# Kernel optimization log

Measured on AMD Instinct MI355X. Metric: run time of the kernel, lower is better.

The kernel has to match this reference:

```python
import jax, jax.numpy as jnp
import numpy as np

B, N, HID, NH = 8, 1024, 1024, 16
HD = HID // NH  # head_dim = 64
MLP = 4 * HID
EPS = 1e-6


def _xavier(key, fan_in, fan_out):
    lim = np.sqrt(6.0 / (fan_in + fan_out))
    return jax.random.uniform(key, (fan_in, fan_out), jnp.float32, -lim, lim)


def setup_inputs() -> dict:
    key = jax.random.key(0)
    ks = jax.random.split(key, 10)
    return {
        "x": jax.random.normal(ks[0], (B, N, HID), jnp.float32),
        "c": jax.random.normal(ks[1], (B, HID), jnp.float32),
        "w_ada": _xavier(ks[2], HID, 6 * HID), "b_ada": jnp.zeros((6 * HID,), jnp.float32),
        "wq": _xavier(ks[3], HID, HID), "bq": jnp.zeros((HID,), jnp.float32),
        "wk": _xavier(ks[4], HID, HID), "bk": jnp.zeros((HID,), jnp.float32),
        "wv": _xavier(ks[5], HID, HID), "bv": jnp.zeros((HID,), jnp.float32),
        "wo": _xavier(ks[6], HID, HID), "bo": jnp.zeros((HID,), jnp.float32),
        "w1": _xavier(ks[7], HID, MLP), "b1": jnp.zeros((MLP,), jnp.float32),
        "w2": _xavier(ks[8], MLP, HID), "b2": jnp.zeros((HID,), jnp.float32),
    }


def _ln(t):
    # LayerNorm, elementwise_affine=False, eps=1e-6
    mu = jnp.mean(t, axis=-1, keepdims=True)
    var = jnp.mean(jnp.square(t - mu), axis=-1, keepdims=True)
    return (t - mu) * jax.lax.rsqrt(var + EPS)


def _modulate(t, shift, scale):
    return t * (1.0 + scale[:, None, :]) + shift[:, None, :]


def reference(x, c, w_ada, b_ada, wq, bq, wk, bk, wv, bv, wo, bo, w1, b1, w2, b2):
    cmod = jax.nn.silu(c) @ w_ada + b_ada  # [B, 6*HID]
    sh_msa, sc_msa, g_msa, sh_mlp, sc_mlp, g_mlp = jnp.split(cmod, 6, axis=-1)

    xm = _modulate(_ln(x), sh_msa, sc_msa)  # [B, N, HID]
    q = (xm @ wq + bq).reshape(B, N, NH, HD)
    k = (xm @ wk + bk).reshape(B, N, NH, HD)
    v = (xm @ wv + bv).reshape(B, N, NH, HD)

    # NOTE: original scales by 1/head_dim (not 1/sqrt(head_dim)), fp32 softmax
    scores = jnp.einsum('bihd,bjhd->bhij', q, k) / HD
    attn = jax.nn.softmax(scores.astype(jnp.float32), axis=-1)
    out = jnp.einsum('bhij,bjhd->bihd', attn, v).astype(v.dtype)
    out = out.reshape(B, N, HID) @ wo + bo

    x = x + g_msa[:, None, :] * out

    xm2 = _modulate(_ln(x), sh_mlp, sc_mlp)
    h = jax.nn.gelu(xm2 @ w1 + b1, approximate=False)  # nn.GELU default = exact
    mlp_out = h @ w2 + b2
    return x + g_mlp[:, None, :] * mlp_out
```

## Files before the change

kernel.cpp:

```cpp
#include <hip/hip_runtime.h>
#include <hip/hip_bf16.h>
#include <cstdint>


typedef __bf16 bf16;
typedef __attribute__((ext_vector_type(8))) __bf16 bf16x8;
typedef __attribute__((ext_vector_type(4))) __bf16 bf16x4;
typedef __attribute__((ext_vector_type(4))) float f32x4;

#define SEQ   1024
#define NHID  1024
#define NHEAD 16
#define HDIM  64
#define CMS   6144

#define GLD16(gp, lp)                                                  \
  __builtin_amdgcn_global_load_lds(                                    \
      (const __attribute__((address_space(1))) void*)(gp),             \
      (__attribute__((address_space(3))) void*)(lp), 16, 0, 0)

template <int N> __device__ __forceinline__ void vmwait() {
  if constexpr (N == 0)      asm volatile("s_waitcnt vmcnt(0)" ::: "memory");
  else if constexpr (N == 4) asm volatile("s_waitcnt vmcnt(4)" ::: "memory");
  else if constexpr (N == 6) asm volatile("s_waitcnt vmcnt(6)" ::: "memory");
}

#define BAR()                                                          \
  { asm volatile("" ::: "memory");                                     \
    __builtin_amdgcn_s_barrier();                                      \
    asm volatile("" ::: "memory"); }

#define LGKM0() asm volatile("s_waitcnt lgkmcnt(0)" ::: "memory")

struct TP4 { const float* s[4]; bf16* d[4]; };

__global__ __launch_bounds__(256) void transpose_conv4(TP4 p)
{
  __shared__ float tile[32][33];
  const float* __restrict__ src = p.s[blockIdx.z];
  bf16* __restrict__ dst = p.d[blockIdx.z];
  int n0 = blockIdx.x * 32, k0 = blockIdx.y * 32;
  int tx = threadIdx.x & 31, ty = threadIdx.x >> 5;
#pragma unroll
  for (int i = 0; i < 32; i += 8)
    tile[ty + i][tx] = src[(size_t)(k0 + ty + i) * 1024 + n0 + tx];
  __syncthreads();
#pragma unroll
  for (int i = 0; i < 32; i += 8)
    dst[(size_t)(n0 + ty + i) * 1024 + k0 + tx] = (bf16)tile[tx][ty + i];
}

__global__ __launch_bounds__(256) void transpose_conv(
    const float* __restrict__ src, bf16* __restrict__ dst, int K, int N)
{
  __shared__ float tile[32][33];
  int n0 = blockIdx.x * 32, k0 = blockIdx.y * 32;
  int tx = threadIdx.x & 31, ty = threadIdx.x >> 5;
#pragma unroll
  for (int i = 0; i < 32; i += 8)
    tile[ty + i][tx] = src[(size_t)(k0 + ty + i) * N + n0 + tx];
  __syncthreads();
#pragma unroll
  for (int i = 0; i < 32; i += 8)
    dst[(size_t)(n0 + ty + i) * K + k0 + tx] = (bf16)tile[tx][ty + i];
}

__global__ __launch_bounds__(256) void ada_kernel(
    const float* __restrict__ c, const float* __restrict__ w_ada,
    const float* __restrict__ b_ada, float* __restrict__ cmod)
{
  __shared__ float cs[1024];
  int b = blockIdx.y;
  int col = blockIdx.x * 256 + threadIdx.x;
  for (int i = threadIdx.x; i < 1024; i += 256) {
    float cv = c[b * 1024 + i];
    cs[i] = cv / (1.0f + __expf(-cv));
  }
  __syncthreads();
  float acc = b_ada[col];
#pragma unroll 8
  for (int kk = 0; kk < 1024; kk++)
    acc += cs[kk] * w_ada[(size_t)kk * CMS + col];
  cmod[b * CMS + col] = acc;
}

__global__ __launch_bounds__(256) void ln_mod(
    const float* __restrict__ x, const float* __restrict__ cmod,
    bf16* __restrict__ out, int sh_off, int sc_off)
{
  int row = blockIdx.x, b = row >> 10, tid = threadIdx.x;
  const float4* xr = (const float4*)(x + (size_t)row * NHID);
  float4 v = xr[tid];
  float s  = v.x + v.y + v.z + v.w;
  float s2 = v.x * v.x + v.y * v.y + v.z * v.z + v.w * v.w;
#pragma unroll
  for (int off = 32; off; off >>= 1) {
    s  += __shfl_xor(s, off);
    s2 += __shfl_xor(s2, off);
  }
  __shared__ float red1[4], red2[4];
  int wave = tid >> 6, lane = tid & 63;
  if (lane == 0) { red1[wave] = s; red2[wave] = s2; }
  __syncthreads();
  float S  = red1[0] + red1[1] + red1[2] + red1[3];
  float S2 = red2[0] + red2[1] + red2[2] + red2[3];
  float mean = S * (1.0f / NHID);
  float var  = S2 * (1.0f / NHID) - mean * mean;
  float rs   = rsqrtf(var + 1e-6f);
  const float4* shp = (const float4*)(cmod + b * CMS + sh_off);
  const float4* scp = (const float4*)(cmod + b * CMS + sc_off);
  float4 sh4 = shp[tid], sc4 = scp[tid];
  bf16x4 o4;
  o4[0] = (bf16)((v.x - mean) * rs * (1.0f + sc4.x) + sh4.x);
  o4[1] = (bf16)((v.y - mean) * rs * (1.0f + sc4.y) + sh4.y);
  o4[2] = (bf16)((v.z - mean) * rs * (1.0f + sc4.z) + sh4.z);
  o4[3] = (bf16)((v.w - mean) * rs * (1.0f + sc4.w) + sh4.w);
  *(bf16x4*)(out + (size_t)row * NHID + tid * 4) = o4;
}

template <int EPI, int BN>
__global__ __launch_bounds__(512, 2) void gemm8(
    const bf16* __restrict__ A, const bf16* __restrict__ Bt,
    const float* __restrict__ bias, const float* __restrict__ bias2,
    const float* __restrict__ bias3,
    bf16* __restrict__ outb, bf16* __restrict__ outb2,
    bf16* __restrict__ outb3, float* __restrict__ outf,
    const float* __restrict__ cmod, int gate_off,
    const float* __restrict__ resid,
    int N, int K)
{
  constexpr int BNH   = BN / 2;
  constexpr int LB    = BNH / 64;
  constexpr int MF    = BN / 64;
  constexpr int WC    = BN / 64;
  constexpr int WRS   = 256 / (8 / WC) / 2;
  constexpr int VMN   = (LB == 2) ? 6 : 4;
  constexpr int BOFF  = 65536;
  constexpr int BBUF  = BNH * 256;
  constexpr int BHALF = BNH * 128;

  extern __shared__ __align__(16) char smem[];

  const int tid  = threadIdx.x;
  const int xcd  = blockIdx.x & 7;
  const int slot = blockIdx.x >> 3;
  const int by   = xcd * 4 + (slot & 3);
  const int bx   = slot >> 2;
  const int bm = by * 256, bn = bx * BN;

  const int wave = tid >> 6, lane = tid & 63;
  const int wr = wave / WC, wc = wave % WC;
  const int l16 = lane & 15, q4 = lane >> 4;

  const int rq = tid >> 3;
  const int ch = ((tid & 7) ^ (rq & 7)) * 8;
  const int wbase = (tid & 448) * 16;

  const int aRowB = (wr * WRS + l16) * 128;
  const int bRowB = (wc * 32 + l16) * 128;
  const int slotB = (q4 ^ (l16 & 7)) * 16;

  f32x4 acc[2][2][MF][2];
#pragma unroll
  for (int a0 = 0; a0 < 2; a0++)
#pragma unroll
    for (int a1 = 0; a1 < 2; a1++)
#pragma unroll
      for (int a2 = 0; a2 < MF; a2++)
#pragma unroll
        for (int a3 = 0; a3 < 2; a3++) acc[a0][a1][a2][a3] = (f32x4)0.0f;

  auto stA = [&](int buf, int half, int T) {
    const bf16* g = A + (size_t)(bm + half * 128 + rq) * K + T * 64 + ch;
    char* l = smem + buf * 32768 + half * 16384 + wbase;
    GLD16(g, l);
    GLD16(g + (size_t)64 * K, l + 8192);
  };
  auto stB = [&](int buf, int half, int T) {
    const bf16* g = Bt + (size_t)(bn + half * BNH + rq) * K + T * 64 + ch;
    char* l = smem + BOFF + buf * BBUF + half * BHALF + wbase;
    GLD16(g, l);
    if constexpr (LB == 2) { GLD16(g + (size_t)64 * K, l + 8192); }
  };

#define RDA(BUF, QM, FR)                                                   \
  { const char* ab_ = smem + (BUF) * 32768 + (QM) * 16384 + aRowB;         \
    _Pragma("unroll")                                                      \
    for (int ks = 0; ks < 2; ks++) {                                       \
      const int sb_ = slotB ^ (ks * 64);                                   \
      _Pragma("unroll")                                                    \
      for (int mf = 0; mf < MF; mf++)                                      \
        FR[ks][mf] = *(const bf16x8*)(ab_ + mf * 2048 + sb_);              \
    } }

#define RDB(BUF, QN, FR)                                                   \
  { const char* bb_ = smem + BOFF + (BUF) * BBUF + (QN) * BHALF + bRowB;   \
    _Pragma("unroll")                                                      \
    for (int ks = 0; ks < 2; ks++) {                                       \
      const int sb_ = slotB ^ (ks * 64);                                   \
      _Pragma("unroll")                                                    \
      for (int nf = 0; nf < 2; nf++)                                       \
        FR[ks][nf] = *(const bf16x8*)(bb_ + nf * 2048 + sb_);              \
    } }

#define MM(QM, QN, AF, BF)                                                 \
  { __builtin_amdgcn_s_setprio(1);                                         \
    _Pragma("unroll")                                                      \
    for (int mf = 0; mf < MF; mf++)                                        \
      _Pragma("unroll")                                                    \
      for (int nf = 0; nf < 2; nf++) {                                     \
        acc[QM][QN][mf][nf] = __builtin_amdgcn_mfma_f32_16x16x32_bf16(     \
            AF[0][mf], BF[0][nf], acc[QM][QN][mf][nf], 0, 0, 0);           \
        acc[QM][QN][mf][nf] = __builtin_amdgcn_mfma_f32_16x16x32_bf16(     \
            AF[1][mf], BF[1][nf], acc[QM][QN][mf][nf], 0, 0, 0);           \
      }                                                                    \
    __builtin_amdgcn_s_setprio(0); }

  const int NT = K >> 6, NI = NT >> 1;

  bf16x8 afr[2][MF], bfr0[2][2], bfr1[2][2];

  stA(0, 0, 0); stB(0, 0, 0); stB(0, 1, 0); stA(0, 1, 0);
  stA(1, 0, 1); stB(1, 0, 1); stB(1, 1, 1);
  vmwait<VMN>();
  BAR();

  for (int i = 0; i < NI; ++i) {
    const int t = 2 * i;
    const int u2 = (t + 2 < NT) ? t + 2 : NT - 2;
    const int u3 = (t + 3 < NT) ? t + 3 : NT - 1;
    RDA(0, 0, afr); RDB(0, 0, bfr0);
    stA(1, 1, t + 1);
    BAR(); LGKM0();
    MM(0, 0, afr, bfr0);
    BAR();
    RDB(0, 1, bfr1);
    stA(0, 0, u2);
    BAR(); LGKM0();
    MM(0, 1, afr, bfr1);
    BAR();
    RDA(0, 1, afr);
    stB(0, 0, u2);
    BAR(); LGKM0();
    MM(1, 1, afr, bfr1);
    BAR();
    stB(0, 1, u2);
    vmwait<VMN>();
    BAR();
    MM(1, 0, afr, bfr0);
    BAR();
    RDA(1, 0, afr); RDB(1, 0, bfr0);
    stA(0, 1, u2);
    BAR(); LGKM0();
    MM(0, 0, afr, bfr0);
    BAR();
    RDB(1, 1, bfr1);
    stA(1, 0, u3);
    BAR(); LGKM0();
    MM(0, 1, afr, bfr1);
    BAR();
    RDA(1, 1, afr);
    stB(1, 0, u3);
    BAR(); LGKM0();
    MM(1, 1, afr, bfr1);
    BAR();
    stB(1, 1, u3);
    vmwait<VMN>();
    BAR();
    MM(1, 0, afr, bfr0);
    BAR();
  }
  vmwait<0>();
#undef RDA
#undef RDB
#undef MM

  const int colBase = bn + wc * 32 + l16;
  const int rowBase = bm + wr * WRS + q4 * 4;
#pragma unroll
  for (int qm = 0; qm < 2; qm++)
#pragma unroll
  for (int qn = 0; qn < 2; qn++)
#pragma unroll
  for (int mf = 0; mf < MF; mf++)
#pragma unroll
  for (int nf = 0; nf < 2; nf++) {
    const int col  = colBase + qn * BNH + nf * 16;
    const int row0 = rowBase + qm * 128 + mf * 16;
    f32x4 v = acc[qm][qn][mf][nf];
    if constexpr (EPI == 5) {
      const int sel = bn >> 10;
      const float* bp = (sel == 0) ? bias : (sel == 1) ? bias2 : bias3;
      const int colq = col & 1023;
      const float bcol = bp[colq];
      if (sel == 2) {
        bf16x4 o4;
#pragma unroll
        for (int r = 0; r < 4; r++) o4[r] = (bf16)(v[r] + bcol);
        const int bidx = row0 >> 10;
        *(bf16x4*)(outb3 + ((size_t)bidx * NHID + colq) * SEQ +
                   (row0 & 1023)) = o4;
      } else {
        bf16* qk = (sel == 0) ? outb : outb2;
#pragma unroll
        for (int r = 0; r < 4; r++)
          qk[(size_t)(row0 + r) * 1024 + colq] = (bf16)(v[r] + bcol);
      }
    } else if constexpr (EPI == 2) {
      const float bcol = bias[col];
#pragma unroll
      for (int r = 0; r < 4; r++) {
        float val = v[r] + bcol;
        float u2g = 2.0f * val * (0.7978845608f + 0.0356774081f * val * val);
        float e = __expf(u2g);
        float th = 1.0f - 2.0f / (e + 1.0f);
        outb[(size_t)(row0 + r) * N + col] = (bf16)(0.5f * val * (1.0f + th));
      }
    } else {
      const float bcol = bias[col];
#pragma unroll
      for (int r = 0; r < 4; r++) {
        const int row = row0 + r;
        const float gg = cmod[(row >> 10) * CMS + gate_off + col];
        outf[(size_t)row * N + col] =
            resid[(size_t)row * N + col] + gg * (v[r] + bcol);
      }
    }
  }
}

__global__ __launch_bounds__(512) void attn_mfma(
    const bf16* __restrict__ q, const bf16* __restrict__ k,
    const bf16* __restrict__ vt, bf16* __restrict__ o)
{
  __shared__ __align__(16) bf16 Ks[64 * 64];
  __shared__ __align__(16) bf16 Vs[64 * 64];
  __shared__ __align__(16) bf16 Ps[8][32 * 72];

  int bid = blockIdx.x;
  int qt = bid & 3, h = (bid >> 2) & 15, b = bid >> 6;
  int tid = threadIdx.x, wave = tid >> 6, lane = tid & 63;
  int quad = lane >> 4, l16 = lane & 15;
  int qbase = qt * 256 + wave * 32;

  bf16x8 qf[2][2];
  const bf16* qp = q + ((size_t)(b * SEQ + qbase)) * NHID + h * HDIM;
#pragma unroll
  for (int nt = 0; nt < 2; nt++)
#pragma unroll
    for (int kk = 0; kk < 2; kk++) {
      bf16x8 t = *(const bf16x8*)(qp + (size_t)(nt * 16 + l16) * NHID +
                                  kk * 32 + quad * 8);
#pragma unroll
      for (int j = 0; j < 8; j++) t[j] = (bf16)((float)t[j] * 0.015625f);
      qf[nt][kk] = t;
    }

  f32x4 oacc[4][2];
#pragma unroll
  for (int mt = 0; mt < 4; mt++)
#pragma unroll
    for (int nt = 0; nt < 2; nt++) oacc[mt][nt] = (f32x4)0.0f;
  float m_[2] = {-3.0e38f, -3.0e38f}, l_[2] = {0.0f, 0.0f};

  const bf16* kb = k + ((size_t)(b * SEQ)) * NHID + h * HDIM;
  const bf16* vb = vt + ((size_t)(b * NHID + h * HDIM)) * SEQ;

  const int sr0 = tid >> 3, sc0 = tid & 7;
  const int cg0 = (sc0 ^ (sr0 & 7)) * 8;
  bf16* lk0 = Ks + (size_t)(tid & 448) * 8;
  bf16* lv0 = Vs + (size_t)(tid & 448) * 8;

  for (int kt = 0; kt < 16; kt++) {
    __syncthreads();
    GLD16(kb + (size_t)(kt * 64 + sr0) * NHID + cg0, lk0);
    GLD16(vb + (size_t)sr0 * SEQ + kt * 64 + cg0, lv0);
    __syncthreads();

    f32x4 sacc[4][2];
#pragma unroll
    for (int mt = 0; mt < 4; mt++)
#pragma unroll
      for (int nt = 0; nt < 2; nt++) sacc[mt][nt] = (f32x4)0.0f;
#pragma unroll
    for (int kk = 0; kk < 2; kk++) {
      bf16x8 kf[4];
#pragma unroll
      for (int mt = 0; mt < 4; mt++) {
        int row = mt * 16 + l16;
        kf[mt] = *(const bf16x8*)(Ks + row * 64 +
                                  (((kk * 4 + quad) ^ (row & 7)) * 8));
      }
#pragma unroll
      for (int mt = 0; mt < 4; mt++)
#pragma unroll
        for (int nt = 0; nt < 2; nt++)
          sacc[mt][nt] = __builtin_amdgcn_mfma_f32_16x16x32_bf16(
              kf[mt], qf[nt][kk], sacc[mt][nt], 0, 0, 0);
    }

    float alpha[2];
#pragma unroll
    for (int nt = 0; nt < 2; nt++) {
      float tm = -3.0e38f;
#pragma unroll
      for (int mt = 0; mt < 4; mt++)
#pragma unroll
        for (int r = 0; r < 4; r++) tm = fmaxf(tm, sacc[mt][nt][r]);
      tm = fmaxf(tm, __shfl_xor(tm, 16));
      tm = fmaxf(tm, __shfl_xor(tm, 32));
      float mn = fmaxf(m_[nt], tm);
      alpha[nt] = __expf(m_[nt] - mn);
      m_[nt] = mn;
      float ts = 0.0f;
#pragma unroll
      for (int mt = 0; mt < 4; mt++) {
        bf16x4 pv;
#pragma unroll
        for (int r = 0; r < 4; r++) {
          float p = __expf(sacc[mt][nt][r] - mn);
          ts += p;
          pv[r] = (bf16)p;
        }
        *(bf16x4*)(&Ps[wave][(nt * 16 + l16) * 72 + mt * 16 + quad * 4]) = pv;
      }
      ts += __shfl_xor(ts, 16);
      ts += __shfl_xor(ts, 32);
      l_[nt] = l_[nt] * alpha[nt] + ts;
    }
#pragma unroll
    for (int mt = 0; mt < 4; mt++)
#pragma unroll
      for (int nt = 0; nt < 2; nt++)
#pragma unroll
        for (int r = 0; r < 4; r++) oacc[mt][nt][r] *= alpha[nt];

    __asm__ volatile("s_waitcnt lgkmcnt(0)" ::: "memory");

#pragma unroll
    for (int kk = 0; kk < 2; kk++) {
      bf16x8 vf[4], pf[2];
#pragma unroll
      for (int mt = 0; mt < 4; mt++) {
        int row = mt * 16 + l16;
        vf[mt] = *(const bf16x8*)(Vs + row * 64 +
                                  (((kk * 4 + quad) ^ (row & 7)) * 8));
      }
#pragma unroll
      for (int nt = 0; nt < 2; nt++)
        pf[nt] = *(const bf16x8*)(&Ps[wave][(nt * 16 + l16) * 72 +
                                            kk * 32 + quad * 8]);
#pragma unroll
      for (int mt = 0; mt < 4; mt++)
#pragma unroll
        for (int nt = 0; nt < 2; nt++)
          oacc[mt][nt] = __builtin_amdgcn_mfma_f32_16x16x32_bf16(
              vf[mt], pf[nt], oacc[mt][nt], 0, 0, 0);
    }
  }

#pragma unroll
  for (int nt = 0; nt < 2; nt++) {
    float rl = 1.0f / l_[nt];
#pragma unroll
    for (int mt = 0; mt < 4; mt++) {
      bf16x4 o4;
#pragma unroll
      for (int r = 0; r < 4; r++) o4[r] = (bf16)(oacc[mt][nt][r] * rl);
      *(bf16x4*)(o + ((size_t)(b * SEQ + qbase + nt * 16 + l16)) * NHID +
                 h * HDIM + mt * 16 + quad * 4) = o4;
    }
  }
}

#define OFF_CMOD 0u
#define OFF_WQT  196608u
#define OFF_WKT  (OFF_WQT + 2097152u)
#define OFF_WVT  (OFF_WKT + 2097152u)
#define OFF_WOT  (OFF_WVT + 2097152u)
#define OFF_W1T  (OFF_WOT + 2097152u)
#define OFF_W2T  (OFF_W1T + 8388608u)
#define OFF_X2   (OFF_W2T + 8388608u)
#define OFF_XM2  (OFF_X2  + 33554432u)
#define OFF_POOL (OFF_XM2 + 16777216u)

extern "C" void kernel_launch(void* const* d_in, const int* in_sizes, int n_in,
                              void* d_out, int out_size, void* d_ws, size_t ws_size,
                              hipStream_t stream)
{
  const float* x     = (const float*)d_in[0];
  const float* c     = (const float*)d_in[1];
  const float* w_ada = (const float*)d_in[2];
  const float* b_ada = (const float*)d_in[3];
  const float* wq = (const float*)d_in[4];  const float* bq = (const float*)d_in[5];
  const float* wk = (const float*)d_in[6];  const float* bk = (const float*)d_in[7];
  const float* wv = (const float*)d_in[8];  const float* bv = (const float*)d_in[9];
  const float* wo = (const float*)d_in[10]; const float* bo = (const float*)d_in[11];
  const float* w1 = (const float*)d_in[12]; const float* b1 = (const float*)d_in[13];
  const float* w2 = (const float*)d_in[14]; const float* b2 = (const float*)d_in[15];
  float* out = (float*)d_out;
  char* ws = (char*)d_ws;

  float* cmod = (float*)(ws + OFF_CMOD);
  bf16* wqT = (bf16*)(ws + OFF_WQT);
  bf16* wkT = (bf16*)(ws + OFF_WKT);
  bf16* wvT = (bf16*)(ws + OFF_WVT);
  bf16* woT = (bf16*)(ws + OFF_WOT);
  bf16* w1T = (bf16*)(ws + OFF_W1T);
  bf16* w2T = (bf16*)(ws + OFF_W2T);
  float* x2 = (float*)(ws + OFF_X2);
  bf16* xm2 = (bf16*)(ws + OFF_XM2);
  bf16* xm  = (bf16*)(ws + OFF_POOL);
  bf16* qb  = (bf16*)(ws + OFF_POOL + 16777216u);
  bf16* kb  = (bf16*)(ws + OFF_POOL + 33554432u);
  bf16* vtb = (bf16*)(ws + OFF_POOL + 50331648u);
  bf16* ob  = xm;
  bf16* hb  = xm;

  static bool attr_set = false;
  if (!attr_set) {
    hipFuncSetAttribute(reinterpret_cast<const void*>(&gemm8<5, 128>),
                        hipFuncAttributeMaxDynamicSharedMemorySize, 98304);
    hipFuncSetAttribute(reinterpret_cast<const void*>(&gemm8<1, 128>),
                        hipFuncAttributeMaxDynamicSharedMemorySize, 98304);
    hipFuncSetAttribute(reinterpret_cast<const void*>(&gemm8<2, 256>),
                        hipFuncAttributeMaxDynamicSharedMemorySize, 131072);
    hipFuncSetAttribute(reinterpret_cast<const void*>(&gemm8<3, 128>),
                        hipFuncAttributeMaxDynamicSharedMemorySize, 98304);
    attr_set = true;
  }

  TP4 tp;
  tp.s[0] = wq; tp.s[1] = wk; tp.s[2] = wv; tp.s[3] = wo;
  tp.d[0] = wqT; tp.d[1] = wkT; tp.d[2] = wvT; tp.d[3] = woT;
  transpose_conv4<<<dim3(32, 32, 4), 256, 0, stream>>>(tp);
  transpose_conv<<<dim3(128, 32), 256, 0, stream>>>(w1, w1T, 1024, 4096);
  transpose_conv<<<dim3(32, 128), 256, 0, stream>>>(w2, w2T, 4096, 1024);

  ada_kernel<<<dim3(24, 8), 256, 0, stream>>>(c, w_ada, b_ada, cmod);

  ln_mod<<<8192, 256, 0, stream>>>(x, cmod, xm, 0, 1024);

  gemm8<5, 128><<<768, 512, 98304, stream>>>(
      xm, wqT, bq, bk, bv, qb, kb, vtb, nullptr, nullptr, 0, nullptr,
      1024, 1024);

  attn_mfma<<<512, 512, 0, stream>>>(qb, kb, vtb, ob);

  gemm8<1, 128><<<256, 512, 98304, stream>>>(
      ob, woT, bo, nullptr, nullptr, nullptr, nullptr, nullptr, x2,
      cmod, 2048, x, 1024, 1024);

  ln_mod<<<8192, 256, 0, stream>>>(x2, cmod, xm2, 3072, 4096);

  gemm8<2, 256><<<512, 512, 131072, stream>>>(
      xm2, w1T, b1, nullptr, nullptr, hb, nullptr, nullptr, nullptr,
      nullptr, 0, nullptr, 4096, 1024);

  gemm8<3, 128><<<256, 512, 98304, stream>>>(
      hb, w2T, b2, nullptr, nullptr, nullptr, nullptr, nullptr, out,
      cmod, 5120, x2, 1024, 4096);
}
```

Measured before the change: 542.6 us.

## Simplify GEMM pipeline to per-tile double buffer and drop BN=256 variant

The GEMM kernel drops its BN template parameter and its finely interleaved 8-phase ping-pong schedule. It now uses a simpler loop that processes one K-tile per iteration, does a full buffer reload with two barriers per tile, and always uses a 256x128 tile. The MLP up-projection now launches 1024 blocks of the smaller tile instead of 512 blocks of 256x256, using less shared memory. This trades the finer overlap of loads and MFMA work, plus the higher reuse of the larger tile, for simpler code and more blocks.

After: 551.1 us. No clear change (+1.6%).

```diff
diff --git a/kernel.cpp b/kernel.cpp
--- a/kernel.cpp
+++ b/kernel.cpp
@@ -21,7 +21,6 @@
 
 template <int N> __device__ __forceinline__ void vmwait() {
   if constexpr (N == 0)      asm volatile("s_waitcnt vmcnt(0)" ::: "memory");
-  else if constexpr (N == 4) asm volatile("s_waitcnt vmcnt(4)" ::: "memory");
   else if constexpr (N == 6) asm volatile("s_waitcnt vmcnt(6)" ::: "memory");
 }
 
@@ -118,7 +117,7 @@
   *(bf16x4*)(out + (size_t)row * NHID + tid * 4) = o4;
 }
 
-template <int EPI, int BN>
+template <int EPI>
 __global__ __launch_bounds__(512, 2) void gemm8(
     const bf16* __restrict__ A, const bf16* __restrict__ Bt,
     const float* __restrict__ bias, const float* __restrict__ bias2,
@@ -129,15 +128,7 @@
     const float* __restrict__ resid,
     int N, int K)
 {
-  constexpr int BNH   = BN / 2;
-  constexpr int LB    = BNH / 64;
-  constexpr int MF    = BN / 64;
-  constexpr int WC    = BN / 64;
-  constexpr int WRS   = 256 / (8 / WC) / 2;
-  constexpr int VMN   = (LB == 2) ? 6 : 4;
-  constexpr int BOFF  = 65536;
-  constexpr int BBUF  = BNH * 256;
-  constexpr int BHALF = BNH * 128;
+  constexpr int BOFF = 65536;
 
   extern __shared__ __align__(16) char smem[];
 
@@ -146,55 +137,54 @@
   const int slot = blockIdx.x >> 3;
   const int by   = xcd * 4 + (slot & 3);
   const int bx   = slot >> 2;
-  const int bm = by * 256, bn = bx * BN;
+  const int bm = by * 256, bn = bx * 128;
 
   const int wave = tid >> 6, lane = tid & 63;
-  const int wr = wave / WC, wc = wave % WC;
+  const int wr = wave >> 1, wc = wave & 1;
   const int l16 = lane & 15, q4 = lane >> 4;
 
   const int rq = tid >> 3;
   const int ch = ((tid & 7) ^ (rq & 7)) * 8;
   const int wbase = (tid & 448) * 16;
 
-  const int aRowB = (wr * WRS + l16) * 128;
+  const int aRowB = (wr * 32 + l16) * 128;
   const int bRowB = (wc * 32 + l16) * 128;
   const int slotB = (q4 ^ (l16 & 7)) * 16;
 
-  f32x4 acc[2][2][MF][2];
+  f32x4 acc[2][2][2][2];
 #pragma unroll
   for (int a0 = 0; a0 < 2; a0++)
 #pragma unroll
     for (int a1 = 0; a1 < 2; a1++)
 #pragma unroll
-      for (int a2 = 0; a2 < MF; a2++)
+      for (int a2 = 0; a2 < 2; a2++)
 #pragma unroll
         for (int a3 = 0; a3 < 2; a3++) acc[a0][a1][a2][a3] = (f32x4)0.0f;
 
-  auto stA = [&](int buf, int half, int T) {
+  auto stA = [&](int p, int half, int T) {
     const bf16* g = A + (size_t)(bm + half * 128 + rq) * K + T * 64 + ch;
-    char* l = smem + buf * 32768 + half * 16384 + wbase;
+    char* l = smem + p * 32768 + half * 16384 + wbase;
     GLD16(g, l);
     GLD16(g + (size_t)64 * K, l + 8192);
   };
-  auto stB = [&](int buf, int half, int T) {
-    const bf16* g = Bt + (size_t)(bn + half * BNH + rq) * K + T * 64 + ch;
-    char* l = smem + BOFF + buf * BBUF + half * BHALF + wbase;
+  auto stB = [&](int p, int half, int T) {
+    const bf16* g = Bt + (size_t)(bn + half * 64 + rq) * K + T * 64 + ch;
+    char* l = smem + BOFF + p * 16384 + half * 8192 + wbase;
     GLD16(g, l);
-    if constexpr (LB == 2) { GLD16(g + (size_t)64 * K, l + 8192); }
   };
 
-#define RDA(BUF, QM, FR)                                                   \
-  { const char* ab_ = smem + (BUF) * 32768 + (QM) * 16384 + aRowB;         \
+#define RDA(P, QM, FR)                                                     \
+  { const char* ab_ = smem + (P) * 32768 + (QM) * 16384 + aRowB;           \
     _Pragma("unroll")                                                      \
     for (int ks = 0; ks < 2; ks++) {                                       \
       const int sb_ = slotB ^ (ks * 64);                                   \
       _Pragma("unroll")                                                    \
-      for (int mf = 0; mf < MF; mf++)                                      \
+      for (int mf = 0; mf < 2; mf++)                                       \
         FR[ks][mf] = *(const bf16x8*)(ab_ + mf * 2048 + sb_);              \
     } }
 
-#define RDB(BUF, QN, FR)                                                   \
-  { const char* bb_ = smem + BOFF + (BUF) * BBUF + (QN) * BHALF + bRowB;   \
+#define RDB(P, QN, FR)                                                     \
+  { const char* bb_ = smem + BOFF + (P) * 16384 + (QN) * 8192 + bRowB;     \
     _Pragma("unroll")                                                      \
     for (int ks = 0; ks < 2; ks++) {                                       \
       const int sb_ = slotB ^ (ks * 64);                                   \
@@ -206,7 +196,7 @@
 #define MM(QM, QN, AF, BF)                                                 \
   { __builtin_amdgcn_s_setprio(1);                                         \
     _Pragma("unroll")                                                      \
-    for (int mf = 0; mf < MF; mf++)                                        \
+    for (int mf = 0; mf < 2; mf++)                                         \
       _Pragma("unroll")                                                    \
       for (int nf = 0; nf < 2; nf++) {                                     \
         acc[QM][QN][mf][nf] = __builtin_amdgcn_mfma_f32_16x16x32_bf16(     \
@@ -216,59 +206,28 @@
       }                                                                    \
     __builtin_amdgcn_s_setprio(0); }
 
-  const int NT = K >> 6, NI = NT >> 1;
-
-  bf16x8 afr[2][MF], bfr0[2][2], bfr1[2][2];
+  const int NT = K >> 6;
+
+  bf16x8 afr[2][2], bfr0[2][2], bfr1[2][2];
 
   stA(0, 0, 0); stB(0, 0, 0); stB(0, 1, 0); stA(0, 1, 0);
-  stA(1, 0, 1); stB(1, 0, 1); stB(1, 1, 1);
-  vmwait<VMN>();
+  stA(1, 0, 1); stB(1, 0, 1); stB(1, 1, 1); stA(1, 1, 1);
+  vmwait<6>();
   BAR();
 
-  for (int i = 0; i < NI; ++i) {
-    const int t = 2 * i;
-    const int u2 = (t + 2 < NT) ? t + 2 : NT - 2;
-    const int u3 = (t + 3 < NT) ? t + 3 : NT - 1;
-    RDA(0, 0, afr); RDB(0, 0, bfr0);
-    stA(1, 1, t + 1);
-    BAR(); LGKM0();
-    MM(0, 0, afr, bfr0);
+  for (int t = 0; t < NT; ++t) {
+    const int p = t & 1;
+    const int T = (t + 2 < NT) ? t + 2 : t;
+    RDA(p, 0, afr); RDB(p, 0, bfr0); RDB(p, 1, bfr1);
+    LGKM0();
+    MM(0, 0, afr, bfr0); MM(0, 1, afr, bfr1);
+    RDA(p, 1, afr);
+    LGKM0();
     BAR();
-    RDB(0, 1, bfr1);
-    stA(0, 0, u2);
-    BAR(); LGKM0();
-    MM(0, 1, afr, bfr1);
+    stA(p, 0, T); stB(p, 0, T); stB(p, 1, T); stA(p, 1, T);
+    vmwait<6>();
     BAR();
-    RDA(0, 1, afr);
-    stB(0, 0, u2);
-    BAR(); LGKM0();
-    MM(1, 1, afr, bfr1);
-    BAR();
-    stB(0, 1, u2);
-    vmwait<VMN>();
-    BAR();
-    MM(1, 0, afr, bfr0);
-    BAR();
-    RDA(1, 0, afr); RDB(1, 0, bfr0);
-    stA(0, 1, u2);
-    BAR(); LGKM0();
-    MM(0, 0, afr, bfr0);
-    BAR();
-    RDB(1, 1, bfr1);
-    stA(1, 0, u3);
-    BAR(); LGKM0();
-    MM(0, 1, afr, bfr1);
-    BAR();
-    RDA(1, 1, afr);
-    stB(1, 0, u3);
-    BAR(); LGKM0();
-    MM(1, 1, afr, bfr1);
-    BAR();
-    stB(1, 1, u3);
-    vmwait<VMN>();
-    BAR();
-    MM(1, 0, afr, bfr0);
-    BAR();
+    MM(1, 1, afr, bfr1); MM(1, 0, afr, bfr0);
   }
   vmwait<0>();
 #undef RDA
@@ -276,16 +235,16 @@
 #undef MM
 
   const int colBase = bn + wc * 32 + l16;
-  const int rowBase = bm + wr * WRS + q4 * 4;
+  const int rowBase = bm + wr * 32 + q4 * 4;
 #pragma unroll
   for (int qm = 0; qm < 2; qm++)
 #pragma unroll
   for (int qn = 0; qn < 2; qn++)
 #pragma unroll
-  for (int mf = 0; mf < MF; mf++)
+  for (int mf = 0; mf < 2; mf++)
 #pragma unroll
   for (int nf = 0; nf < 2; nf++) {
-    const int col  = colBase + qn * BNH + nf * 16;
+    const int col  = colBase + qn * 64 + nf * 16;
     const int row0 = rowBase + qm * 128 + mf * 16;
     f32x4 v = acc[qm][qn][mf][nf];
     if constexpr (EPI == 5) {
@@ -519,13 +478,13 @@
 
   static bool attr_set = false;
   if (!attr_set) {
-    hipFuncSetAttribute(reinterpret_cast<const void*>(&gemm8<5, 128>),
+    hipFuncSetAttribute(reinterpret_cast<const void*>(&gemm8<5>),
                         hipFuncAttributeMaxDynamicSharedMemorySize, 98304);
-    hipFuncSetAttribute(reinterpret_cast<const void*>(&gemm8<1, 128>),
+    hipFuncSetAttribute(reinterpret_cast<const void*>(&gemm8<1>),
                         hipFuncAttributeMaxDynamicSharedMemorySize, 98304);
-    hipFuncSetAttribute(reinterpret_cast<const void*>(&gemm8<2, 256>),
-                        hipFuncAttributeMaxDynamicSharedMemorySize, 131072);
-    hipFuncSetAttribute(reinterpret_cast<const void*>(&gemm8<3, 128>),
+    hipFuncSetAttribute(reinterpret_cast<const void*>(&gemm8<2>),
+                        hipFuncAttributeMaxDynamicSharedMemorySize, 98304);
+    hipFuncSetAttribute(reinterpret_cast<const void*>(&gemm8<3>),
                         hipFuncAttributeMaxDynamicSharedMemorySize, 98304);
     attr_set = true;
   }
@@ -541,23 +500,23 @@
 
   ln_mod<<<8192, 256, 0, stream>>>(x, cmod, xm, 0, 1024);
 
-  gemm8<5, 128><<<768, 512, 98304, stream>>>(
+  gemm8<5><<<768, 512, 98304, stream>>>(
       xm, wqT, bq, bk, bv, qb, kb, vtb, nullptr, nullptr, 0, nullptr,
       1024, 1024);
 
   attn_mfma<<<512, 512, 0, stream>>>(qb, kb, vtb, ob);
 
-  gemm8<1, 128><<<256, 512, 98304, stream>>>(
+  gemm8<1><<<256, 512, 98304, stream>>>(
       ob, woT, bo, nullptr, nullptr, nullptr, nullptr, nullptr, x2,
       cmod, 2048, x, 1024, 1024);
 
   ln_mod<<<8192, 256, 0, stream>>>(x2, cmod, xm2, 3072, 4096);
 
-  gemm8<2, 256><<<512, 512, 131072, stream>>>(
+  gemm8<2><<<1024, 512, 98304, stream>>>(
       xm2, w1T, b1, nullptr, nullptr, hb, nullptr, nullptr, nullptr,
       nullptr, 0, nullptr, 4096, 1024);
 
-  gemm8<3, 128><<<256, 512, 98304, stream>>>(
+  gemm8<3><<<256, 512, 98304, stream>>>(
       hb, w2T, b2, nullptr, nullptr, nullptr, nullptr, nullptr, out,
       cmod, 5120, x2, 1024, 4096);
 }
```

## Double-buffer K/V tiles in attention and split-K the adaLN projection

Applied to the files above, without the earlier changes.

The attention kernel now keeps two LDS buffers for the K and V tiles. It issues the async global-to-LDS load for the next key tile before computing on the current one, and drops one of the two per-iteration barriers. The adaLN modulation GEMV is split four ways along K across a new grid dimension and accumulated with float atomics into a buffer zeroed by a memset. This raises block count for that small kernel. The cost is extra LDS per attention block, an additional memset launch, and non-deterministic summation order in cmod.

New measurement: 503.1 us. 1.08x faster.

```diff
diff --git a/kernel.cpp b/kernel.cpp
--- a/kernel.cpp
+++ b/kernel.cpp
@@ -69,19 +69,20 @@
     const float* __restrict__ c, const float* __restrict__ w_ada,
     const float* __restrict__ b_ada, float* __restrict__ cmod)
 {
-  __shared__ float cs[1024];
-  int b = blockIdx.y;
-  int col = blockIdx.x * 256 + threadIdx.x;
-  for (int i = threadIdx.x; i < 1024; i += 256) {
-    float cv = c[b * 1024 + i];
-    cs[i] = cv / (1.0f + __expf(-cv));
+  __shared__ float cs[256];
+  const int b  = blockIdx.y;
+  const int k0 = blockIdx.z * 256;
+  const int col = blockIdx.x * 256 + threadIdx.x;
+  {
+    float cv = c[b * 1024 + k0 + threadIdx.x];
+    cs[threadIdx.x] = cv / (1.0f + __expf(-cv));
   }
   __syncthreads();
-  float acc = b_ada[col];
+  float acc = (blockIdx.z == 0) ? b_ada[col] : 0.0f;
 #pragma unroll 8
-  for (int kk = 0; kk < 1024; kk++)
-    acc += cs[kk] * w_ada[(size_t)kk * CMS + col];
-  cmod[b * CMS + col] = acc;
+  for (int kk = 0; kk < 256; kk++)
+    acc += cs[kk] * w_ada[(size_t)(k0 + kk) * CMS + col];
+  atomicAdd(&cmod[b * CMS + col], acc);
 }
 
 __global__ __launch_bounds__(256) void ln_mod(
@@ -333,8 +334,8 @@
     const bf16* __restrict__ q, const bf16* __restrict__ k,
     const bf16* __restrict__ vt, bf16* __restrict__ o)
 {
-  __shared__ __align__(16) bf16 Ks[64 * 64];
-  __shared__ __align__(16) bf16 Vs[64 * 64];
+  __shared__ __align__(16) bf16 Ks[2][64 * 64];
+  __shared__ __align__(16) bf16 Vs[2][64 * 64];
   __shared__ __align__(16) bf16 Ps[8][32 * 72];
 
   int bid = blockIdx.x;
@@ -368,14 +369,19 @@
 
   const int sr0 = tid >> 3, sc0 = tid & 7;
   const int cg0 = (sc0 ^ (sr0 & 7)) * 8;
-  bf16* lk0 = Ks + (size_t)(tid & 448) * 8;
-  bf16* lv0 = Vs + (size_t)(tid & 448) * 8;
+  const int lofs = (tid & 448) * 8;
+
+  auto stage = [&](int p, int kt) {
+    GLD16(kb + (size_t)(kt * 64 + sr0) * NHID + cg0, &Ks[p][0] + lofs);
+    GLD16(vb + (size_t)sr0 * SEQ + kt * 64 + cg0, &Vs[p][0] + lofs);
+  };
+
+  stage(0, 0);
+  __syncthreads();
 
   for (int kt = 0; kt < 16; kt++) {
-    __syncthreads();
-    GLD16(kb + (size_t)(kt * 64 + sr0) * NHID + cg0, lk0);
-    GLD16(vb + (size_t)sr0 * SEQ + kt * 64 + cg0, lv0);
-    __syncthreads();
+    const int p = kt & 1;
+    if (kt + 1 < 16) stage(p ^ 1, kt + 1);
 
     f32x4 sacc[4][2];
 #pragma unroll
@@ -388,7 +394,7 @@
 #pragma unroll
       for (int mt = 0; mt < 4; mt++) {
         int row = mt * 16 + l16;
-        kf[mt] = *(const bf16x8*)(Ks + row * 64 +
+        kf[mt] = *(const bf16x8*)(&Ks[p][0] + row * 64 +
                                   (((kk * 4 + quad) ^ (row & 7)) * 8));
       }
 #pragma unroll
@@ -418,9 +424,9 @@
         bf16x4 pv;
 #pragma unroll
         for (int r = 0; r < 4; r++) {
-          float p = __expf(sacc[mt][nt][r] - mn);
-          ts += p;
-          pv[r] = (bf16)p;
+          float p2 = __expf(sacc[mt][nt][r] - mn);
+          ts += p2;
+          pv[r] = (bf16)p2;
         }
         *(bf16x4*)(&Ps[wave][(nt * 16 + l16) * 72 + mt * 16 + quad * 4]) = pv;
       }
@@ -443,7 +449,7 @@
 #pragma unroll
       for (int mt = 0; mt < 4; mt++) {
         int row = mt * 16 + l16;
-        vf[mt] = *(const bf16x8*)(Vs + row * 64 +
+        vf[mt] = *(const bf16x8*)(&Vs[p][0] + row * 64 +
                                   (((kk * 4 + quad) ^ (row & 7)) * 8));
       }
 #pragma unroll
@@ -457,6 +463,8 @@
           oacc[mt][nt] = __builtin_amdgcn_mfma_f32_16x16x32_bf16(
               vf[mt], pf[nt], oacc[mt][nt], 0, 0, 0);
     }
+
+    __syncthreads();
   }
 
 #pragma unroll
@@ -537,7 +545,8 @@
   transpose_conv<<<dim3(128, 32), 256, 0, stream>>>(w1, w1T, 1024, 4096);
   transpose_conv<<<dim3(32, 128), 256, 0, stream>>>(w2, w2T, 4096, 1024);
 
-  ada_kernel<<<dim3(24, 8), 256, 0, stream>>>(c, w_ada, b_ada, cmod);
+  hipMemsetAsync(cmod, 0, 196608u, stream);
+  ada_kernel<<<dim3(24, 8, 4), 256, 0, stream>>>(c, w_ada, b_ada, cmod);
 
   ln_mod<<<8192, 256, 0, stream>>>(x, cmod, xm, 0, 1024);
 
```
